# Performance work log

Measured on AMD Instinct MI355X. Metric: run time of the kernel, lower is better.

The kernel has to match this reference:

```python
import jax, jax.numpy as jnp
import numpy as np

EPS = 1e-15          # min-norm clamp (matches torch min_norm)
BALL_EPS = 4e-3      # float32 Poincare ball boundary eps
C = 1.0              # curvature for every layer


def _artanh(x):
    x = jnp.clip(x, -1.0 + 1e-7, 1.0 - 1e-7)
    return 0.5 * jnp.log((1.0 + x) / (1.0 - x))


def _norm(x):
    return jnp.maximum(jnp.linalg.norm(x, axis=-1, keepdims=True), EPS)


def proj(x, c):
    # clip points to stay inside the ball of radius (1-eps)/sqrt(c)
    n = _norm(x)
    maxnorm = (1.0 - BALL_EPS) / jnp.sqrt(c)
    return jnp.where(n > maxnorm, x / n * maxnorm, x)


def expmap0(u, c):
    sc = jnp.sqrt(c)
    n = _norm(u)
    return jnp.tanh(sc * n) * u / (sc * n)


def logmap0(p, c):
    sc = jnp.sqrt(c)
    n = _norm(p)
    return _artanh(sc * n) * p / (sc * n)


def mobius_add(x, y, c):
    x2 = jnp.sum(x * x, axis=-1, keepdims=True)
    y2 = jnp.sum(y * y, axis=-1, keepdims=True)
    xy = jnp.sum(x * y, axis=-1, keepdims=True)
    num = (1.0 + 2.0 * c * xy + c * y2) * x + (1.0 - c * x2) * y
    den = 1.0 + 2.0 * c * xy + (c ** 2) * x2 * y2
    return num / jnp.maximum(den, EPS)


def mobius_matvec(W, x, c):
    # torch HypLinear: mx = x @ W.T
    sc = jnp.sqrt(c)
    xn = _norm(x)
    mx = x @ W.T
    mxn = _norm(mx)
    res = jnp.tanh(mxn / xn * _artanh(sc * xn)) * mx / (mxn * sc)
    zero = jnp.all(mx == 0.0, axis=-1, keepdims=True)
    return jnp.where(zero, jnp.zeros((), dtype=res.dtype), res)


def hgc_layer(h, src, dst, w, W, b, c_in, c_out, n_nodes):
    # HypLinear
    mv = proj(mobius_matvec(W, h, c_in), c_in)
    hb = proj(expmap0(b[None, :], c_in), c_in)
    h = proj(mobius_add(mv, hb, c_in), c_in)
    # HypAgg: spmm in the tangent space at the origin
    xt = logmap0(h, c_in)                                  # [N, D]
    msg = w[:, None] * xt[src]                             # [E, D]
    agg = jax.ops.segment_sum(msg, dst, num_segments=n_nodes)
    h = proj(expmap0(agg, c_in), c_in)
    # HypAct: relu in tangent space, re-map with c_out
    xt = jax.nn.relu(logmap0(h, c_in))
    return proj(expmap0(xt, c_out), c_out)


def setup_inputs() -> dict:
    key = jax.random.key(0)
    k = jax.random.split(key, 8)
    N, E, F, D = 80000, 1280000, 256, 64
    x = jax.random.normal(k[0], (N, F), dtype=jnp.float32)
    src = jax.random.randint(k[1], (E,), 0, N)
    dst = jax.random.randint(k[2], (E,), 0, N)
    edge_weight = jax.random.uniform(k[3], (E,), dtype=jnp.float32)
    W1 = jax.random.normal(k[4], (D, F), dtype=jnp.float32) / np.sqrt(F)
    b1 = jax.random.normal(k[5], (D,), dtype=jnp.float32) * 0.01
    W2 = jax.random.normal(k[6], (D, D), dtype=jnp.float32) / np.sqrt(D)
    b2 = jax.random.normal(k[7], (D,), dtype=jnp.float32) * 0.01
    return {"x": x, "src": src, "dst": dst, "edge_weight": edge_weight,
            "W1": W1, "b1": b1, "W2": W2, "b2": b2}


def reference(x, src, dst, edge_weight, W1, b1, W2, b2):
    n_nodes = x.shape[0]
    # encode(): proj_tan0 is identity on the Poincare ball
    h = proj(expmap0(x, C), C)
    h = hgc_layer(h, src, dst, edge_weight, W1, b1, C, C, n_nodes)
    h = hgc_layer(h, src, dst, edge_weight, W2, b2, C, C, n_nodes)
    return h
```

## Files before the change

kernel.cpp:

```cpp
#include <hip/hip_runtime.h>


#define EPSV 1e-15f
#define MAXN 0.996f

typedef unsigned short bfu;
typedef __attribute__((ext_vector_type(8))) short v8s;
typedef __attribute__((ext_vector_type(4))) float v4f;

__device__ __forceinline__ bfu f2b(float f) {
    unsigned int u;
    __builtin_memcpy(&u, &f, sizeof(u));
    u += 0x7fffu + ((u >> 16) & 1u);
    return (bfu)(u >> 16);
}

__device__ __forceinline__ float b2f(bfu s) {
    unsigned int u = ((unsigned int)s) << 16;
    float f;
    __builtin_memcpy(&f, &u, sizeof(f));
    return f;
}

__device__ __forceinline__ float uplo(unsigned int u) {
// ... 226 lines not shown
        acc3 = __builtin_amdgcn_mfma_f32_16x16x32_bf16(a, *(const v8s*)(wb + 48 * 256), acc3, 0, 0, 0);
    }
    layer1_tail(nodeBase, m, q, usq, hbv, y2, acc0, acc1, acc2, acc3, xtb);
}

__global__ __launch_bounds__(256) void hgA_zero_i32(int* __restrict__ p, int n) {
    int stride = gridDim.x * blockDim.x;
    for (int i = blockIdx.x * blockDim.x + threadIdx.x; i < n; i += stride) p[i] = 0;
}

__global__ __launch_bounds__(256) void hgA_count(
    const int* __restrict__ dst, int* __restrict__ deg, int E) {
    int stride = gridDim.x * blockDim.x;
    for (int e = blockIdx.x * blockDim.x + threadIdx.x; e < E; e += stride)
        atomicAdd(&deg[dst[e]], 1);
}

__global__ __launch_bounds__(256) void hgA_count_rank_l1(
    const int* __restrict__ dst, int* __restrict__ deg, int* __restrict__ rank,
    int E, int nf, int nl,
    const float* __restrict__ x, const bfu* __restrict__ w1b,
    const float* __restrict__ b1v, bfu* __restrict__ xtb, int N)
{
    const int b = blockIdx.x;
    const int mn = nf < nl ? nf : nl;
    bool isC; int idx;
    if (b < 2 * mn) { isC = !(b & 1); idx = b >> 1; }
    else            { isC = (nf > nl); idx = mn + (b - 2 * mn); }
    if (isC) {
        int e0 = (idx * 256 + threadIdx.x) * 4;
        if (e0 + 4 <= E) {
            int4 d4 = *(const int4*)(dst + e0);
            int4 r4;
            r4.x = atomicAdd(&deg[d4.x], 1);
            r4.y = atomicAdd(&deg[d4.y], 1);
            r4.z = atomicAdd(&deg[d4.z], 1);
            r4.w = atomicAdd(&deg[d4.w], 1);
            *(int4*)(rank + e0) = r4;
        } else if (e0 < E) {
            for (int e = e0; e < E; ++e) rank[e] = atomicAdd(&deg[dst[e]], 1);
        }
    } else {
        layer1_body(idx, threadIdx.x, x, w1b, b1v, xtb, N);
    }
}

__global__ __launch_bounds__(256) void hgA_count_xcvt(
    const int* __restrict__ dst, int* __restrict__ deg, int* __restrict__ rank,
    int E, int nf,
    const float* __restrict__ x, bfu* __restrict__ xb, float* __restrict__ usqt,
    int nc, int N)
{
    const int b = blockIdx.x;
    const int mn = nf < nc ? nf : nc;
    bool isC; int idx;
    if (b < 2 * mn) { isC = !(b & 1); idx = b >> 1; }
    else            { isC = (nf > nc); idx = mn + (b - 2 * mn); }
    if (isC) {
        int e0 = (idx * 256 + threadIdx.x) * 4;
        if (e0 + 4 <= E) {
            int4 d4 = *(const int4*)(dst + e0);
            int4 r4;
            r4.x = atomicAdd(&deg[d4.x], 1);
            r4.y = atomicAdd(&deg[d4.y], 1);
            r4.z = atomicAdd(&deg[d4.z], 1);
            r4.w = atomicAdd(&deg[d4.w], 1);
            *(int4*)(rank + e0) = r4;
        } else if (e0 < E) {
            for (int e = e0; e < E; ++e) rank[e] = atomicAdd(&deg[dst[e]], 1);
        }
    } else {
        const int lane = threadIdx.x & 63, wv = threadIdx.x >> 6;
        const int nodeBase = (idx * 4 + wv) * 16;
        if (nodeBase >= N) return;
        const int m = lane & 15, q = lane >> 4;
        const float* arow = x + (size_t)(nodeBase + m) * 256 + q * 8;
        bfu* orow = xb + (size_t)(nodeBase + m) * 256 + q * 8;
        float usq = 0.0f;
#pragma unroll
        for (int s = 0; s < 8; ++s) {
            float af[8];
            *(float4*)(af)     = *(const float4*)(arow + s * 32);
            *(float4*)(af + 4) = *(const float4*)(arow + s * 32 + 4);
#pragma unroll
            for (int j = 0; j < 8; ++j) usq = fmaf(af[j], af[j], usq);
            *(v8s*)(orow + s * 32) = cvt8(af);
        }
        usq += __shfl_xor(usq, 16, 64);
        usq += __shfl_xor(usq, 32, 64);
        if (lane < 16 && nodeBase + lane < N) usqt[nodeBase + lane] = usq;
    }
}

__global__ __launch_bounds__(256) void hgA_scan1(
    const int* __restrict__ deg, int* __restrict__ rowst,
    int* __restrict__ bsum, int N, int NBr,
    const bfu* __restrict__ xb, const float* __restrict__ usqt,
    const bfu* __restrict__ w1b, const float* __restrict__ b1v,
    bfu* __restrict__ xtb, int NL)
{
    if (blockIdx.x >= NBr) {
        int vb = blockIdx.x - NBr;
        if (vb < NL) layer1b_body(vb, threadIdx.x, xb, usqt, w1b, b1v, xtb, N);
        return;
    }
    __shared__ int wsum[4];
    const int tid = threadIdx.x, lane = tid & 63, wv = tid >> 6;
    const int base = blockIdx.x * 1024 + tid * 4;
    int v0 = 0, v1 = 0, v2 = 0, v3 = 0;
    if (base + 4 <= N) {
        int4 d4 = *(const int4*)(deg + base);
        v0 = d4.x; v1 = d4.y; v2 = d4.z; v3 = d4.w;
    } else {
        if (base + 0 < N) v0 = deg[base + 0];
        if (base + 1 < N) v1 = deg[base + 1];
        if (base + 2 < N) v2 = deg[base + 2];
        if (base + 3 < N) v3 = deg[base + 3];
    }
    const int tsum = v0 + v1 + v2 + v3;
    int incl = tsum;
#pragma unroll
    for (int o = 1; o < 64; o <<= 1) {
        int nb = __shfl_up(incl, o, 64);
        if (lane >= o) incl += nb;
    }
    if (lane == 63) wsum[wv] = incl;
    __syncthreads();
    int add = 0;
#pragma unroll
    for (int w = 0; w < 4; ++w) { int s = wsum[w]; if (w < wv) add += s; }
    const int excl = add + incl - tsum;
    const int e0 = excl, e1 = e0 + v0, e2 = e1 + v1, e3 = e2 + v2;
    if (base + 4 <= N) {
        *(int4*)(rowst + base) = make_int4(e0, e1, e2, e3);
    } else {
        if (base + 0 < N) rowst[base + 0] = e0;
        if (base + 1 < N) rowst[base + 1] = e1;
        if (base + 2 < N) rowst[base + 2] = e2;
        if (base + 3 < N) rowst[base + 3] = e3;
    }
    if (tid == 255) bsum[blockIdx.x] = add + incl;
}

__global__ __launch_bounds__(64) void hgA_scan2(
    int* __restrict__ bsum, int* __restrict__ tot, int NB)
{
    const int lane = threadIdx.x;
    int run = 0;
    for (int b = 0; b < NB; b += 64) {
        int i = b + lane;
        int v = (i < NB) ? bsum[i] : 0;
        int incl = v;
#pragma unroll
        for (int o = 1; o < 64; o <<= 1) {
            int nb = __shfl_up(incl, o, 64);
            if (lane >= o) incl += nb;
        }
        if (i < NB) bsum[i] = run + incl - v;
        run += __shfl(incl, 63);
    }
    if (lane == 0) *tot = run;
}

__global__ __launch_bounds__(256) void hgA_scan3(
    int* __restrict__ rowst, const int* __restrict__ bsum, int N)
{
    const int base = blockIdx.x * 1024 + threadIdx.x * 4;
    const int off = bsum[blockIdx.x];
    if (base + 4 <= N) {
        int4 r = *(int4*)(rowst + base);
        r.x += off; r.y += off; r.z += off; r.w += off;
        *(int4*)(rowst + base) = r;
    } else {
        for (int i = base; i < N; ++i) rowst[i] += off;
    }
}

__global__ __launch_bounds__(1024) void hgA_scan_l1(
    const int* __restrict__ deg, int* __restrict__ row_start,
    int* __restrict__ cursor, int N,
    const float* __restrict__ x, const bfu* __restrict__ w1b,
    const float* __restrict__ b1v, bfu* __restrict__ xtb, int NL)
{
    if (blockIdx.x != 0) {
        int vb = (blockIdx.x - 1) * 4 + (threadIdx.x >> 8);
        if (vb < NL) layer1_body(vb, threadIdx.x & 255, x, w1b, b1v, xtb, N);
        return;
    }
    __shared__ int wsum[16];
    __shared__ int srun;
    const int tid = threadIdx.x, lane = tid & 63, wv = tid >> 6;
    if (tid == 0) srun = 0;
    __syncthreads();
    for (int base = 0; base < N; base += 1024) {
        int i = base + tid;
        int v = (i < N) ? deg[i] : 0;
        int incl = v;
#pragma unroll
        for (int o = 1; o < 64; o <<= 1) {
            int nbr = __shfl_up(incl, o, 64);
            if (lane >= o) incl += nbr;
        }
        if (lane == 63) wsum[wv] = incl;
        __syncthreads();
        int add = 0;
#pragma unroll
        for (int w = 0; w < 16; ++w) { int s = wsum[w]; if (w < wv) add += s; }
        int excl = srun + add + incl - v;
        if (i < N) { row_start[i] = excl; cursor[i] = excl; }
        __syncthreads();
        if (tid == 1023) srun += add + incl;
        __syncthreads();
    }
    if (tid == 0) row_start[N] = srun;
}

__global__ __launch_bounds__(256) void hgA_fill_layer1(
    const int* __restrict__ src, const int* __restrict__ dst,
    const float* __restrict__ ew, int* __restrict__ cursor,
    int2* __restrict__ csr, int E, int fillBlocks,
    const float* __restrict__ x, const bfu* __restrict__ w1b,
    const float* __restrict__ b1v, bfu* __restrict__ xtb, int N)
{
    const int b = blockIdx.x;
    if (b < fillBlocks) {
        int stride = fillBlocks * blockDim.x;
        for (int e = b * blockDim.x + threadIdx.x; e < E; e += stride) {
            int d = dst[e];
            int slot = atomicAdd(&cursor[d], 1);
            csr[slot] = make_int2(src[e], f2i(ew[e]));
        }
    } else {
        layer1_body(b - fillBlocks, threadIdx.x, x, w1b, b1v, xtb, N);
    }
}

__global__ __launch_bounds__(256) void hgA_fillr_layer1(
    const int* __restrict__ src, const int* __restrict__ dst,
    const float* __restrict__ ew, const int* __restrict__ rank,
    const int* __restrict__ row_start, int2* __restrict__ csr,
    int E, int nf, int nl, int l1off,
    const float* __restrict__ x, const bfu* __restrict__ w1b,
    const float* __restrict__ b1v, bfu* __restrict__ xtb, int N)
{
    const int b = blockIdx.x;
    const int mn = nf < nl ? nf : nl;
    bool isFill; int idx;
    if (b < 2 * mn) { isFill = !(b & 1); idx = b >> 1; }
    else            { isFill = (nf > nl); idx = mn + (b - 2 * mn); }
    if (isFill) {
        int e0 = (idx * 256 + threadIdx.x) * 4;
        if (e0 + 4 <= E) {
            int4  d4 = *(const int4*)(dst + e0);
            int4  s4 = *(const int4*)(src + e0);
            int4  r4 = *(const int4*)(rank + e0);
            float4 w4 = *(const float4*)(ew + e0);
            csr[row_start[d4.x] + r4.x] = make_int2(s4.x, f2i(w4.x));
            csr[row_start[d4.y] + r4.y] = make_int2(s4.y, f2i(w4.y));
            csr[row_start[d4.z] + r4.z] = make_int2(s4.z, f2i(w4.z));
            csr[row_start[d4.w] + r4.w] = make_int2(s4.w, f2i(w4.w));
        } else if (e0 < E) {
            for (int e = e0; e < E; ++e)
                csr[row_start[dst[e]] + rank[e]] = make_int2(src[e], f2i(ew[e]));
        }
    } else {
        layer1_body(l1off + idx, threadIdx.x, x, w1b, b1v, xtb, N);
    }
}

__global__ __launch_bounds__(256) void hgA_fillr_l1b(
    const int* __restrict__ src, const int* __restrict__ dst,
    const float* __restrict__ ew, const int* __restrict__ rank,
    const int* __restrict__ row_start, int2* __restrict__ csr,
    int E, int nf, int nl, int l1off,
    const bfu* __restrict__ xb, const float* __restrict__ usqt,
    const bfu* __restrict__ w1b, const float* __restrict__ b1v,
    bfu* __restrict__ xtb, int N)
{
    const int b = blockIdx.x;
    const int mn = nf < nl ? nf : nl;
    bool isFill; int idx;
    if (b < 2 * mn) { isFill = !(b & 1); idx = b >> 1; }
    else            { isFill = (nf > nl); idx = mn + (b - 2 * mn); }
    if (isFill) {
        int e0 = (idx * 256 + threadIdx.x) * 4;
        if (e0 + 4 <= E) {
            int4  d4 = *(const int4*)(dst + e0);
            int4  s4 = *(const int4*)(src + e0);
            int4  r4 = *(const int4*)(rank + e0);
            float4 w4 = *(const float4*)(ew + e0);
            csr[row_start[d4.x] + r4.x] = make_int2(s4.x, f2i(w4.x));
            csr[row_start[d4.y] + r4.y] = make_int2(s4.y, f2i(w4.y));
            csr[row_start[d4.z] + r4.z] = make_int2(s4.z, f2i(w4.z));
            csr[row_start[d4.w] + r4.w] = make_int2(s4.w, f2i(w4.w));
        } else if (e0 < E) {
            for (int e = e0; e < E; ++e)
                csr[row_start[dst[e]] + rank[e]] = make_int2(src[e], f2i(ew[e]));
        }
    } else {
        layer1b_body(l1off + idx, threadIdx.x, xb, usqt, w1b, b1v, xtb, N);
    }
}

#define GACC_QUAD(T64, CSR, N0, N1, LANE, T0, T1, T2, T3)                      \
    {                                                                          \
        const int sl_ = (LANE) & 15, p_ = (LANE) >> 4;                         \
        float a0x=0.f,a0y=0.f,a0z=0.f,a0w=0.f;                                 \
        float a1x=0.f,a1y=0.f,a1z=0.f,a1w=0.f;                                 \
        float a2x=0.f,a2y=0.f,a2z=0.f,a2w=0.f;                                 \
        float a3x=0.f,a3y=0.f,a3z=0.f,a3w=0.f;                                 \
        for (int base = (N0); base < (N1); base += 64) {                       \
            int cnt = (N1) - base; if (cnt > 64) cnt = 64;                     \
            int sL = 0; float wL = 0.0f;                                       \
            if ((LANE) < cnt) { int2 rec = (CSR)[base + (LANE)];               \
                                sL = rec.x; wL = i2f(rec.y); }                 \
            int j = 0;                                                         \
            for (; j + 16 <= cnt; j += 16) {                                   \
                int   s0 = __shfl(sL, j      + p_, 64);                        \
                int   s1 = __shfl(sL, j +  4 + p_, 64);                        \
                int   s2 = __shfl(sL, j +  8 + p_, 64);                        \
                int   s3 = __shfl(sL, j + 12 + p_, 64);                        \
                float w0 = __shfl(wL, j      + p_, 64);                        \
                float w1 = __shfl(wL, j +  4 + p_, 64);                        \
                float w2 = __shfl(wL, j +  8 + p_, 64);                        \
                float w3 = __shfl(wL, j + 12 + p_, 64);                        \
                uint2 u0 = (T64)[(size_t)s0 * 16 + sl_];                       \
                uint2 u1 = (T64)[(size_t)s1 * 16 + sl_];                       \
                uint2 u2 = (T64)[(size_t)s2 * 16 + sl_];                       \
                uint2 u3 = (T64)[(size_t)s3 * 16 + sl_];                       \
                a0x = fmaf(w0, uplo(u0.x), a0x); a0y = fmaf(w0, uphi(u0.x), a0y); \
                a0z = fmaf(w0, uplo(u0.y), a0z); a0w = fmaf(w0, uphi(u0.y), a0w); \
                a1x = fmaf(w1, uplo(u1.x), a1x); a1y = fmaf(w1, uphi(u1.x), a1y); \
                a1z = fmaf(w1, uplo(u1.y), a1z); a1w = fmaf(w1, uphi(u1.y), a1w); \
                a2x = fmaf(w2, uplo(u2.x), a2x); a2y = fmaf(w2, uphi(u2.x), a2y); \
                a2z = fmaf(w2, uplo(u2.y), a2z); a2w = fmaf(w2, uphi(u2.y), a2w); \
                a3x = fmaf(w3, uplo(u3.x), a3x); a3y = fmaf(w3, uphi(u3.x), a3y); \
                a3z = fmaf(w3, uplo(u3.y), a3z); a3w = fmaf(w3, uphi(u3.y), a3w); \
            }                                                                  \
            for (; j + 8 <= cnt; j += 8) {                                     \
                int   s0 = __shfl(sL, j     + p_, 64);                         \
                int   s1 = __shfl(sL, j + 4 + p_, 64);                         \
                float w0 = __shfl(wL, j     + p_, 64);                         \
                float w1 = __shfl(wL, j + 4 + p_, 64);                         \
                uint2 u0 = (T64)[(size_t)s0 * 16 + sl_];                       \
                uint2 u1 = (T64)[(size_t)s1 * 16 + sl_];                       \
                a0x = fmaf(w0, uplo(u0.x), a0x); a0y = fmaf(w0, uphi(u0.x), a0y); \
                a0z = fmaf(w0, uplo(u0.y), a0z); a0w = fmaf(w0, uphi(u0.y), a0w); \
                a1x = fmaf(w1, uplo(u1.x), a1x); a1y = fmaf(w1, uphi(u1.x), a1y); \
                a1z = fmaf(w1, uplo(u1.y), a1z); a1w = fmaf(w1, uphi(u1.y), a1w); \
            }                                                                  \
            for (; j < cnt; j += 4) {         \
                int   s = __shfl(sL, j + p_, 64);                              \
                float w = __shfl(wL, j + p_, 64);                              \
                uint2 u = (T64)[(size_t)s * 16 + sl_];                         \
                a0x = fmaf(w, uplo(u.x), a0x); a0y = fmaf(w, uphi(u.x), a0y);  \
                a0z = fmaf(w, uplo(u.y), a0z); a0w = fmaf(w, uphi(u.y), a0w);  \
            }                                                                  \
        }                                                                      \
        T0 = (a0x + a1x) + (a2x + a3x);                                        \
        T1 = (a0y + a1y) + (a2y + a3y);                                        \
        T2 = (a0z + a1z) + (a2z + a3z);                                        \
        T3 = (a0w + a1w) + (a2w + a3w);                                        \
        T0 += __shfl_xor(T0, 16, 64); T0 += __shfl_xor(T0, 32, 64);            \
        T1 += __shfl_xor(T1, 16, 64); T1 += __shfl_xor(T1, 32, 64);            \
        T2 += __shfl_xor(T2, 16, 64); T2 += __shfl_xor(T2, 32, 64);            \
        T3 += __shfl_xor(T3, 16, 64); T3 += __shfl_xor(T3, 32, 64);            \
    }

__global__ __launch_bounds__(256) void hgA_gather(
    const int* __restrict__ row_start, const int2* __restrict__ csr,
    const bfu* __restrict__ xtb, float* __restrict__ agg, int N) {
    const int lane = threadIdx.x & 63, wv = threadIdx.x >> 6;
    const int d = blockIdx.x * 4 + wv;
    if (d >= N) return;
    const uint2* t64 = (const uint2*)xtb;
    const int n0 = row_start[d], n1 = row_start[d + 1];
    float t0, t1, t2, t3;
    GACC_QUAD(t64, csr, n0, n1, lane, t0, t1, t2, t3);
    if ((lane >> 4) == 0)
        *(float4*)(agg + (size_t)d * 64 + 4 * (lane & 15)) =
            make_float4(t0, t1, t2, t3);
}

__global__ __launch_bounds__(256) void hgA_gather_out(
    const int* __restrict__ row_start, const int2* __restrict__ csr,
    const bfu* __restrict__ xtb2, float* __restrict__ out, int N) {
    const int lane = threadIdx.x & 63, wv = threadIdx.x >> 6;
    const int d = blockIdx.x * 4 + wv;
    if (d >= N) return;
    const uint2* t64 = (const uint2*)xtb2;
    const int n0 = row_start[d], n1 = row_start[d + 1];
    float t0, t1, t2, t3;
    GACC_QUAD(t64, csr, n0, n1, lane, t0, t1, t2, t3);
    float ssq = t0*t0 + t1*t1 + t2*t2 + t3*t3;
#pragma unroll
    for (int o = 1; o < 16; o <<= 1) ssq += __shfl_xor(ssq, o, 64);
    float n  = fmaxf(sqrtf(ssq), EPSV);
    float th = tanhf(n);
    float g  = th / n;
    float nh = fmaxf(th, EPSV);
    if (nh > MAXN) { g *= MAXN / nh; nh = MAXN; }
    float lamg = (artanh_(nh) / nh) * g;
    float r0 = fmaxf(lamg * t0, 0.0f);
    float r1 = fmaxf(lamg * t1, 0.0f);
    float r2 = fmaxf(lamg * t2, 0.0f);
    float r3 = fmaxf(lamg * t3, 0.0f);
    float tsq = r0*r0 + r1*r1 + r2*r2 + r3*r3;
#pragma unroll
    for (int o = 1; o < 16; o <<= 1) tsq += __shfl_xor(tsq, o, 64);
    float n2  = fmaxf(sqrtf(tsq), EPSV);
    float th2 = tanhf(n2);
    float g2  = th2 / n2;
    float nh2 = fmaxf(th2, EPSV);
    if (nh2 > MAXN) g2 *= MAXN / nh2;
    if ((lane >> 4) == 0)
        *(float4*)(out + (size_t)d * 64 + 4 * (lane & 15)) =
            make_float4(g2 * r0, g2 * r1, g2 * r2, g2 * r3);
}

__global__ __launch_bounds__(256) void hgA_layer2_mfma(
    const float* __restrict__ agg,
    const bfu* __restrict__ w2b,
    const float* __restrict__ b2v,
    bfu* __restrict__ xtb2, int N)
{
    const int tid = threadIdx.x, lane = tid & 63, wv = tid >> 6;
    const int nodeBase = (blockIdx.x * 4 + wv) * 16;
    if (nodeBase >= N) return;

    float y2;
    float hb = bias_point(b2v, lane, &y2);
    float hbv[4];
#pragma unroll
    for (int t = 0; t < 4; ++t) hbv[t] = __shfl(hb, (lane & 15) + 16 * t);

    const int m = lane & 15, q = lane >> 4;
    const bool rowok = (nodeBase + m) < N;

    float af0[8], af1[8];
    const float* arow = agg + (size_t)(nodeBase + m) * 64 + q * 8;
    if (rowok) {
        *(float4*)(af0)     = *(const float4*)(arow);
        *(float4*)(af0 + 4) = *(const float4*)(arow + 4);
        *(float4*)(af1)     = *(const float4*)(arow + 32);
        *(float4*)(af1 + 4) = *(const float4*)(arow + 36);
    } else {
#pragma unroll
        for (int j = 0; j < 8; ++j) { af0[j] = 0.0f; af1[j] = 0.0f; }
    }
    float asq = 0.0f;
#pragma unroll
    for (int j = 0; j < 8; ++j) {
        asq = fmaf(af0[j], af0[j], asq);
        asq = fmaf(af1[j], af1[j], asq);
    }
    asq += __shfl_xor(asq, 16, 64);
    asq += __shfl_xor(asq, 32, 64);

    float n  = fmaxf(sqrtf(asq), EPSV);
    float th = tanhf(n);
    float g  = th / n;
    float nh = fmaxf(th, EPSV);
    if (nh > MAXN) { g *= MAXN / nh; nh = MAXN; }
    float lamg = (artanh_(nh) / nh) * g;
    float t0[8], t1[8], tsq = 0.0f;
#pragma unroll
    for (int j = 0; j < 8; ++j) {
        t0[j] = fmaxf(lamg * af0[j], 0.0f);
        t1[j] = fmaxf(lamg * af1[j], 0.0f);
        tsq = fmaf(t0[j], t0[j], tsq);
        tsq = fmaf(t1[j], t1[j], tsq);
    }
    tsq += __shfl_xor(tsq, 16, 64);
    tsq += __shfl_xor(tsq, 32, 64);
    float n2  = fmaxf(sqrtf(tsq), EPSV);
    float th2 = tanhf(n2);
    float g2  = th2 / n2;
    float nh2 = fmaxf(th2, EPSV);
    if (nh2 > MAXN) { g2 *= MAXN / nh2; nh2 = MAXN; }
    float xn_m = nh2;
    float x0[8], x1[8];
#pragma unroll
    for (int j = 0; j < 8; ++j) { x0[j] = g2 * t0[j]; x1[j] = g2 * t1[j]; }
    v8s a0 = cvt8(x0), a1 = cvt8(x1);

    v4f acc0 = {0,0,0,0}, acc1 = {0,0,0,0}, acc2 = {0,0,0,0}, acc3 = {0,0,0,0};
    {
        const bfu* wb;
        wb = w2b + (size_t)(m     ) * 64 + q * 8;
        acc0 = __builtin_amdgcn_mfma_f32_16x16x32_bf16(a0, *(const v8s*)(wb),      acc0, 0, 0, 0);
        acc0 = __builtin_amdgcn_mfma_f32_16x16x32_bf16(a1, *(const v8s*)(wb + 32), acc0, 0, 0, 0);
        wb = w2b + (size_t)(m + 16) * 64 + q * 8;
        acc1 = __builtin_amdgcn_mfma_f32_16x16x32_bf16(a0, *(const v8s*)(wb),      acc1, 0, 0, 0);
        acc1 = __builtin_amdgcn_mfma_f32_16x16x32_bf16(a1, *(const v8s*)(wb + 32), acc1, 0, 0, 0);
        wb = w2b + (size_t)(m + 32) * 64 + q * 8;
        acc2 = __builtin_amdgcn_mfma_f32_16x16x32_bf16(a0, *(const v8s*)(wb),      acc2, 0, 0, 0);
        acc2 = __builtin_amdgcn_mfma_f32_16x16x32_bf16(a1, *(const v8s*)(wb + 32), acc2, 0, 0, 0);
        wb = w2b + (size_t)(m + 48) * 64 + q * 8;
        acc3 = __builtin_amdgcn_mfma_f32_16x16x32_bf16(a0, *(const v8s*)(wb),      acc3, 0, 0, 0);
        acc3 = __builtin_amdgcn_mfma_f32_16x16x32_bf16(a1, *(const v8s*)(wb + 32), acc3, 0, 0, 0);
    }

    float P[4], Q[4];
#pragma unroll
    for (int r = 0; r < 4; ++r) {
        float s2 = acc0[r]*acc0[r] + acc1[r]*acc1[r] + acc2[r]*acc2[r] + acc3[r]*acc3[r];
        float sh = acc0[r]*hbv[0] + acc1[r]*hbv[1] + acc2[r]*hbv[2] + acc3[r]*hbv[3];
#pragma unroll
        for (int o = 1; o < 16; o <<= 1) {
            s2 += __shfl_xor(s2, o, 64);
            sh += __shfl_xor(sh, o, 64);
        }
        float xn = __shfl(xn_m, q * 4 + r);
        float mxn = fmaxf(sqrtf(s2), EPSV);
        float rt  = tanhf(mxn / xn * artanh_(xn));
        float k1, x2s, xy;
        if (s2 != 0.0f) {
            k1 = rt / mxn;
            float mvn = fmaxf(fabsf(rt), EPSV);
            if (mvn > MAXN) k1 *= MAXN / mvn;
            float cn = fminf(mvn, MAXN);
            x2s = cn * cn;
            xy  = k1 * sh;
        } else { k1 = 0.0f; x2s = 0.0f; xy = 0.0f; }
        float ca = 1.0f + 2.0f * xy + y2;
        float cb = 1.0f - x2s;
        float den = fmaxf(1.0f + 2.0f * xy + x2s * y2, EPSV);
        float hn2 = ca*ca*x2s + 2.0f*ca*cb*xy + cb*cb*y2;
        float hn = fmaxf(sqrtf(hn2) / den, EPSV);
        float hs = 1.0f;
        if (hn > MAXN) { hs = MAXN / hn; hn = MAXN; }
        float lam = artanh_(hn) / hn;
        P[r] = lam * hs * ca * k1 / den;
        Q[r] = lam * hs * cb / den;
    }
#pragma unroll
    for (int r = 0; r < 4; ++r) {
        int ri = nodeBase + q * 4 + r;
        if (ri < N) {
            bfu* orow = xtb2 + (size_t)ri * 64 + m;
            orow[ 0] = f2b(P[r] * acc0[r] + Q[r] * hbv[0]);
            orow[16] = f2b(P[r] * acc1[r] + Q[r] * hbv[1]);
            orow[32] = f2b(P[r] * acc2[r] + Q[r] * hbv[2]);
            orow[48] = f2b(P[r] * acc3[r] + Q[r] * hbv[3]);
        }
    }
}

__global__ __launch_bounds__(256) void hgA_layer1_fp32(
    const float* __restrict__ x, const float* __restrict__ W1,
    const float* __restrict__ b1v, float* __restrict__ xt, int N)
{
    const int tid = threadIdx.x, lane = tid & 63, wv = tid >> 6;
    const int nodeBase = (blockIdx.x * 4 + wv) * 16;
    if (nodeBase >= N) return;
    float y2;
    float hb = bias_point(b1v, lane, &y2);
    float hbv[4];
#pragma unroll
    for (int t = 0; t < 4; ++t) hbv[t] = __shfl(hb, (lane & 15) + 16 * t);
    const int m = lane & 15, q = lane >> 4;
    v4f acc0 = {0,0,0,0}, acc1 = {0,0,0,0}, acc2 = {0,0,0,0}, acc3 = {0,0,0,0};
    float usq = 0.0f;
    const float* arow = x + (size_t)(nodeBase + m) * 256 + q * 8;
#pragma unroll
    for (int s = 0; s < 8; ++s) {
        float af[8];
        *(float4*)(af)     = *(const float4*)(arow + s * 32);
        *(float4*)(af + 4) = *(const float4*)(arow + s * 32 + 4);
#pragma unroll
        for (int j = 0; j < 8; ++j) usq = fmaf(af[j], af[j], usq);
        v8s a = cvt8(af);
        const float* wbase = W1 + (size_t)m * 256 + s * 32 + q * 8;
        float wf[8];
        *(float4*)(wf) = *(const float4*)(wbase);  *(float4*)(wf+4) = *(const float4*)(wbase+4);
        acc0 = __builtin_amdgcn_mfma_f32_16x16x32_bf16(a, cvt8(wf), acc0, 0, 0, 0);
        *(float4*)(wf) = *(const float4*)(wbase+16*256); *(float4*)(wf+4) = *(const float4*)(wbase+16*256+4);
        acc1 = __builtin_amdgcn_mfma_f32_16x16x32_bf16(a, cvt8(wf), acc1, 0, 0, 0);
        *(float4*)(wf) = *(const float4*)(wbase+32*256); *(float4*)(wf+4) = *(const float4*)(wbase+32*256+4);
        acc2 = __builtin_amdgcn_mfma_f32_16x16x32_bf16(a, cvt8(wf), acc2, 0, 0, 0);
        *(float4*)(wf) = *(const float4*)(wbase+48*256); *(float4*)(wf+4) = *(const float4*)(wbase+48*256+4);
        acc3 = __builtin_amdgcn_mfma_f32_16x16x32_bf16(a, cvt8(wf), acc3, 0, 0, 0);
    }
    usq += __shfl_xor(usq, 16, 64);
    usq += __shfl_xor(usq, 32, 64);
    float P[4], Q[4];
#pragma unroll
    for (int r = 0; r < 4; ++r) {
        float s2 = acc0[r]*acc0[r] + acc1[r]*acc1[r] + acc2[r]*acc2[r] + acc3[r]*acc3[r];
        float sh = acc0[r]*hbv[0] + acc1[r]*hbv[1] + acc2[r]*hbv[2] + acc3[r]*hbv[3];
#pragma unroll
        for (int o = 1; o < 16; o <<= 1) { s2 += __shfl_xor(s2, o, 64); sh += __shfl_xor(sh, o, 64); }
        float usq_r = __shfl(usq, q * 4 + r);
        float n  = fmaxf(sqrtf(usq_r), EPSV);
        float th = tanhf(n);
        float gamma = th / n;
        float xn = fmaxf(th, EPSV);
        if (xn > MAXN) { gamma *= MAXN / xn; xn = MAXN; }
        float mxn = fmaxf(gamma * sqrtf(s2), EPSV);
        float rt  = tanhf(mxn / xn * artanh_(xn));
        float k1, x2s, xy;
        if (s2 != 0.0f) {
            k1 = (rt / mxn) * gamma;
            float mvn = fmaxf(fabsf(rt), EPSV);
            if (mvn > MAXN) k1 *= MAXN / mvn;
            float cn = fminf(mvn, MAXN);
            x2s = cn * cn; xy = k1 * sh;
        } else { k1 = 0.0f; x2s = 0.0f; xy = 0.0f; }
        float ca = 1.0f + 2.0f * xy + y2;
        float cb = 1.0f - x2s;
        float den = fmaxf(1.0f + 2.0f * xy + x2s * y2, EPSV);
        float hn2 = ca*ca*x2s + 2.0f*ca*cb*xy + cb*cb*y2;
        float hn = fmaxf(sqrtf(hn2) / den, EPSV);
        float hs = 1.0f;
        if (hn > MAXN) { hs = MAXN / hn; hn = MAXN; }
        float lam = artanh_(hn) / hn;
        P[r] = lam * hs * ca * k1 / den;
        Q[r] = lam * hs * cb / den;
    }
#pragma unroll
    for (int r = 0; r < 4; ++r) {
        float* orow = xt + (size_t)(nodeBase + q * 4 + r) * 64 + m;
        orow[ 0] = P[r] * acc0[r] + Q[r] * hbv[0];
        orow[16] = P[r] * acc1[r] + Q[r] * hbv[1];
        orow[32] = P[r] * acc2[r] + Q[r] * hbv[2];
        orow[48] = P[r] * acc3[r] + Q[r] * hbv[3];
    }
}

__global__ __launch_bounds__(256) void hgA_scatter(
    const int* __restrict__ src, const int* __restrict__ dst,
    const float* __restrict__ ew,
    const float* __restrict__ xt, float* __restrict__ agg, int E)
{
    const int lane = threadIdx.x & 63;
    const long long wid = ((long long)blockIdx.x * blockDim.x + threadIdx.x) >> 6;
    const long long nw = ((long long)gridDim.x * blockDim.x) >> 6;
    for (long long e = wid; e < E; e += nw) {
        int s = src[e], d = dst[e];
        atomicAdd(&agg[(size_t)d * 64 + lane], ew[e] * xt[(size_t)s * 64 + lane]);
    }
}

__global__ __launch_bounds__(256) void hgA_layer2_fb(
    const float* __restrict__ agg,
    const float* __restrict__ W2, const float* __restrict__ b2v,
    float* __restrict__ xt2, int N)
{
    const int lane = threadIdx.x & 63, wv = threadIdx.x >> 6;
    float y2;
    float hb = bias_point(b2v, lane, &y2);
    const int nw = gridDim.x * 4;
    for (int i = blockIdx.x * 4 + wv; i < N; i += nw) {
        float a = agg[(size_t)i * 64 + lane];
        float xn;
        float x2 = agg_transform(a, &xn);
        float acc = 0.0f;
        const float* Wrow = W2 + (size_t)lane * 64;
        for (int s = 0; s < 64; ++s)
            acc = fmaf(__shfl(x2, s), Wrow[s], acc);
        float o = mobius_tail(acc, xn, hb, y2);
        xt2[(size_t)i * 64 + lane] = o;
    }
}

__global__ __launch_bounds__(256) void hgA_final_fb(
    const float* __restrict__ agg, float* __restrict__ out, int N)
{
    const int lane = threadIdx.x & 63, wv = threadIdx.x >> 6;
    const int nw = gridDim.x * 4;
    for (int i = blockIdx.x * 4 + wv; i < N; i += nw) {
        float a = agg[(size_t)i * 64 + lane];
        float xn;
        float o = agg_transform(a, &xn);
        out[(size_t)i * 64 + lane] = o;
    }
}

extern "C" void kernel_launch(void* const* d_in, const int* in_sizes, int n_in,
                              void* d_out, int out_size, void* d_ws, size_t ws_size,
                              hipStream_t stream)
{
    const float* x  = (const float*)d_in[0];
    const int* src  = (const int*)d_in[1];
    const int* dst  = (const int*)d_in[2];
    const float* ew = (const float*)d_in[3];
    const float* W1 = (const float*)d_in[4];
    const float* b1 = (const float*)d_in[5];
    const float* W2 = (const float*)d_in[6];
    const float* b2 = (const float*)d_in[7];

    const int Dd = in_sizes[5];
    const int Ff = in_sizes[4] / Dd;
    const int N  = in_sizes[0] / Ff;
    const int E  = in_sizes[1];
    const int NW1 = Dd * Ff;
    const int NW2 = Dd * Dd;

    float* out = (float*)d_out;
    float* agg = (float*)d_out;

    const int NB = (N + 1023) / 1024;

    const int blkT = (N + 63) / 64;
    const int blkG = (N + 3) / 4;
    const int blkE4 = (E + 1023) / 1024;
    const int prepG = 128 + (NW1 + 255) / 256 + 1;
    const int n4 = (N * Dd) / 4;

    size_t xtb_b = (size_t)N * Dd * 2;
    size_t xb_b  = (size_t)N * Ff * 2;
    bfu*  xtb   = (bfu*)d_ws;
    bfu*  xbA   = (bfu*)((char*)d_ws + xtb_b);
    float* usqt = (float*)((char*)d_ws + xtb_b + xb_b);
    size_t off1 = xtb_b + xb_b + (size_t)N * 4;
    int*  degA1   = (int*)((char*)d_ws + off1);
    int*  rowstA1 = degA1 + N;
    int*  rankA1  = rowstA1 + (N + 1);
    int*  bsumA1  = rankA1 + E;
    size_t w1_offA1 = (off1 + ((size_t)(2 * N + 1) + (size_t)E + (size_t)NB) * 4 + 15) & ~(size_t)15;
    bfu* w1bA1 = (bfu*)((char*)d_ws + w1_offA1);
    bfu* w2bA1 = w1bA1 + NW1;
    size_t csr_offA1 = (w1_offA1 + (size_t)(NW1 + NW2) * 2 + 7) & ~(size_t)7;
    const size_t needA1 = csr_offA1 + (size_t)E * 8;

    int*  deg    = (int*)((char*)d_ws + xtb_b);
    int*  rowst  = deg + N;
    int*  cursor = rowst + (N + 1);
    int*  rank   = cursor + N;
    int*  bsum   = rank + E;
    size_t wA_off = (xtb_b + ((size_t)(3 * N + 1) + (size_t)E + (size_t)NB) * 4 + 15) & ~(size_t)15;
    bfu* w1bA = (bfu*)((char*)d_ws + wA_off);
    bfu* w2bA = w1bA + NW1;
    size_t csr_offA = (wA_off + (size_t)(NW1 + NW2) * 2 + 7) & ~(size_t)7;
    const size_t needA2 = csr_offA + (size_t)E * 8;

    size_t wB_off = (xtb_b + (size_t)(3 * N + 1) * 4 + 15) & ~(size_t)15;
    bfu* w1bB = (bfu*)((char*)d_ws + wB_off);
    bfu* w2bB = w1bB + NW1;
    size_t csr_offB = (wB_off + (size_t)(NW1 + NW2) * 2 + 7) & ~(size_t)7;
    const size_t needB = csr_offB + (size_t)E * 8;

    if (ws_size >= needA1) {
        int2* csr = (int2*)((char*)d_ws + csr_offA1);
        int L1S = blkT < 192 ? blkT : 192;
        int L1F = blkT - L1S;
        hgA_prep      <<<prepG, 256, 0, stream>>>(degA1, N, W1, W2, w1bA1, w2bA1, NW1, NW2);
        hgA_count_xcvt<<<blkE4 + blkT, 256, 0, stream>>>(
            dst, degA1, rankA1, E, blkE4, x, xbA, usqt, blkT, N);
        hgA_scan1     <<<NB + L1S, 256, 0, stream>>>(
            degA1, rowstA1, bsumA1, N, NB, xbA, usqt, w1bA1, b1, xtb, L1S);
        hgA_scan2     <<<1, 64, 0, stream>>>(bsumA1, rowstA1 + N, NB);
        hgA_scan3     <<<NB, 256, 0, stream>>>(rowstA1, bsumA1, N);
        hgA_fillr_l1b <<<blkE4 + L1F, 256, 0, stream>>>(
            src, dst, ew, rankA1, rowstA1, csr, E, blkE4, L1F, L1S,
            xbA, usqt, w1bA1, b1, xtb, N);
        hgA_gather     <<<blkG, 256, 0, stream>>>(rowstA1, csr, xtb, agg, N);
        hgA_layer2_mfma<<<blkT, 256, 0, stream>>>(agg, w2bA1, b2, xtb, N);
        hgA_gather_out <<<blkG, 256, 0, stream>>>(rowstA1, csr, xtb, out, N);
    } else if (ws_size >= needA2) {
        int2* csr = (int2*)((char*)d_ws + csr_offA);
        int L1C = blkT < 780 ? blkT : 780;
        int L1F = blkT - L1C;
        hgA_prep        <<<prepG, 256, 0, stream>>>(deg, N, W1, W2, w1bA, w2bA, NW1, NW2);
        hgA_count_rank_l1<<<blkE4 + L1C, 256, 0, stream>>>(
            dst, deg, rank, E, blkE4, L1C, x, w1bA, b1, xtb, N);
        hgA_scan1       <<<NB, 256, 0, stream>>>(deg, rowst, bsum, N, NB,
                                                 (const bfu*)xtb, (const float*)deg,
                                                 w1bA, b1, xtb, 0);
        hgA_scan2       <<<1,   64, 0, stream>>>(bsum, rowst + N, NB);
        hgA_scan3       <<<NB, 256, 0, stream>>>(rowst, bsum, N);
        hgA_fillr_layer1<<<blkE4 + L1F, 256, 0, stream>>>(
            src, dst, ew, rank, rowst, csr, E, blkE4, L1F, L1C,
            x, w1bA, b1, xtb, N);
        hgA_gather     <<<blkG, 256, 0, stream>>>(rowst, csr, xtb, agg, N);
        hgA_layer2_mfma<<<blkT, 256, 0, stream>>>(agg, w2bA, b2, xtb, N);
        hgA_gather_out <<<blkG, 256, 0, stream>>>(rowst, csr, xtb, out, N);
    } else if (ws_size >= needB) {
        int2* csr = (int2*)((char*)d_ws + csr_offB);
        const int fillBlocks = 2048;
        hgA_prep       <<<prepG, 256, 0, stream>>>(deg, N, W1, W2, w1bB, w2bB, NW1, NW2);
        hgA_count      <<<2048, 256, 0, stream>>>(dst, deg, E);
        hgA_scan_l1    <<<1,   1024, 0, stream>>>(
            deg, rowst, cursor, N, x, w1bB, b1, xtb, 0);
        hgA_fill_layer1<<<fillBlocks + blkT, 256, 0, stream>>>(
            src, dst, ew, cursor, csr, E, fillBlocks, x, w1bB, b1, xtb, N);
        hgA_gather     <<<blkG, 256, 0, stream>>>(rowst, csr, xtb, agg, N);
        hgA_layer2_mfma<<<blkT, 256, 0, stream>>>(agg, w2bB, b2, xtb, N);
        hgA_gather_out <<<blkG, 256, 0, stream>>>(rowst, csr, xtb, out, N);
    } else {
        float* xt_fb  = (float*)d_out;
        float* agg_fb = (float*)d_ws;
        hgA_layer1_fp32<<<blkT, 256, 0, stream>>>(x, W1, b1, xt_fb, N);
        hgA_zero     <<<1024,  256, 0, stream>>>(agg_fb, n4);
        hgA_scatter  <<<16384, 256, 0, stream>>>(src, dst, ew, xt_fb, agg_fb, E);
        hgA_layer2_fb<<<2048,  256, 0, stream>>>(agg_fb, W2, b2, xt_fb, N);
        hgA_zero     <<<1024,  256, 0, stream>>>(agg_fb, n4);
        hgA_scatter  <<<16384, 256, 0, stream>>>(src, dst, ew, xt_fb, agg_fb, E);
        hgA_final_fb <<<2048,  256, 0, stream>>>(agg_fb, out, N);
    }
}
```

Baseline: 333.4 us.

## Map each 16-lane group to one destination row in the CSR gathers

Both gather kernels now assign one 16-lane group per destination node, so each wave handles four rows. Previously a whole wave handled one row with four 16-lane groups splitting its edges. Each group walks its row's edges serially, eight gathered loads at a time, using two accumulator sets. This removes the cross-group shfl_xor reduction and the idle lanes at the store, and cuts the number of launched blocks by four. In exchange, rows of unequal degree in the same wave now diverge, and each lane runs a longer serial loop.

Measured after the change: 315.2 us. 1.06x faster.

```diff
diff --git a/kernel.cpp b/kernel.cpp
--- a/kernel.cpp
+++ b/kernel.cpp
@@ -552,105 +552,105 @@
     }
 }
 
-#define GACC_QUAD(T64, CSR, N0, N1, LANE, T0, T1, T2, T3)                      \
+#define GACC_G16(T64, CSR, N0, N1, SL, GBASE, AX, AY, AZ, AW)                  \
     {                                                                          \
-        const int sl_ = (LANE) & 15, p_ = (LANE) >> 4;                         \
-        float a0x=0.f,a0y=0.f,a0z=0.f,a0w=0.f;                                 \
-        float a1x=0.f,a1y=0.f,a1z=0.f,a1w=0.f;                                 \
-        float a2x=0.f,a2y=0.f,a2z=0.f,a2w=0.f;                                 \
-        float a3x=0.f,a3y=0.f,a3z=0.f,a3w=0.f;                                 \
-        for (int base = (N0); base < (N1); base += 64) {                       \
-            int cnt = (N1) - base; if (cnt > 64) cnt = 64;                     \
+        float bx=0.f,by=0.f,bz=0.f,bw=0.f;                                     \
+        for (int base = (N0); base < (N1); base += 16) {                       \
+            int cnt = (N1) - base; if (cnt > 16) cnt = 16;                     \
             int sL = 0; float wL = 0.0f;                                       \
-            if ((LANE) < cnt) { int2 rec = (CSR)[base + (LANE)];               \
-                                sL = rec.x; wL = i2f(rec.y); }                 \
+            if ((SL) < cnt) { int2 rec = (CSR)[base + (SL)];                   \
+                              sL = rec.x; wL = i2f(rec.y); }                   \
             int j = 0;                                                         \
-            for (; j + 16 <= cnt; j += 16) {                                   \
-                int   s0 = __shfl(sL, j      + p_, 64);                        \
-                int   s1 = __shfl(sL, j +  4 + p_, 64);                        \
-                int   s2 = __shfl(sL, j +  8 + p_, 64);                        \
-                int   s3 = __shfl(sL, j + 12 + p_, 64);                        \
-                float w0 = __shfl(wL, j      + p_, 64);                        \
-                float w1 = __shfl(wL, j +  4 + p_, 64);                        \
-                float w2 = __shfl(wL, j +  8 + p_, 64);                        \
-                float w3 = __shfl(wL, j + 12 + p_, 64);                        \
-                uint2 u0 = (T64)[(size_t)s0 * 16 + sl_];                       \
-                uint2 u1 = (T64)[(size_t)s1 * 16 + sl_];                       \
-                uint2 u2 = (T64)[(size_t)s2 * 16 + sl_];                       \
-                uint2 u3 = (T64)[(size_t)s3 * 16 + sl_];                       \
-                a0x = fmaf(w0, uplo(u0.x), a0x); a0y = fmaf(w0, uphi(u0.x), a0y); \
-                a0z = fmaf(w0, uplo(u0.y), a0z); a0w = fmaf(w0, uphi(u0.y), a0w); \
-                a1x = fmaf(w1, uplo(u1.x), a1x); a1y = fmaf(w1, uphi(u1.x), a1y); \
-                a1z = fmaf(w1, uplo(u1.y), a1z); a1w = fmaf(w1, uphi(u1.y), a1w); \
-                a2x = fmaf(w2, uplo(u2.x), a2x); a2y = fmaf(w2, uphi(u2.x), a2y); \
-                a2z = fmaf(w2, uplo(u2.y), a2z); a2w = fmaf(w2, uphi(u2.y), a2w); \
-                a3x = fmaf(w3, uplo(u3.x), a3x); a3y = fmaf(w3, uphi(u3.x), a3y); \
-                a3z = fmaf(w3, uplo(u3.y), a3z); a3w = fmaf(w3, uphi(u3.y), a3w); \
+            for (; j + 8 <= cnt; j += 8) {                                     \
+                int   s0 = __shfl(sL, (GBASE)+j  , 64), s1 = __shfl(sL, (GBASE)+j+1, 64); \
+                int   s2 = __shfl(sL, (GBASE)+j+2, 64), s3 = __shfl(sL, (GBASE)+j+3, 64); \
+                int   s4 = __shfl(sL, (GBASE)+j+4, 64), s5 = __shfl(sL, (GBASE)+j+5, 64); \
+                int   s6 = __shfl(sL, (GBASE)+j+6, 64), s7 = __shfl(sL, (GBASE)+j+7, 64); \
+                float w0 = __shfl(wL, (GBASE)+j  , 64), w1 = __shfl(wL, (GBASE)+j+1, 64); \
+                float w2 = __shfl(wL, (GBASE)+j+2, 64), w3 = __shfl(wL, (GBASE)+j+3, 64); \
+                float w4 = __shfl(wL, (GBASE)+j+4, 64), w5 = __shfl(wL, (GBASE)+j+5, 64); \
+                float w6 = __shfl(wL, (GBASE)+j+6, 64), w7 = __shfl(wL, (GBASE)+j+7, 64); \
+                uint2 u0 = (T64)[(size_t)s0 * 16 + (SL)];                      \
+                uint2 u1 = (T64)[(size_t)s1 * 16 + (SL)];                      \
+                uint2 u2 = (T64)[(size_t)s2 * 16 + (SL)];                      \
+                uint2 u3 = (T64)[(size_t)s3 * 16 + (SL)];                      \
+                uint2 u4 = (T64)[(size_t)s4 * 16 + (SL)];                      \
+                uint2 u5 = (T64)[(size_t)s5 * 16 + (SL)];                      \
+                uint2 u6 = (T64)[(size_t)s6 * 16 + (SL)];                      \
+                uint2 u7 = (T64)[(size_t)s7 * 16 + (SL)];                      \
+                AX = fmaf(w0, uplo(u0.x), AX); AY = fmaf(w0, uphi(u0.x), AY);  \
+                AZ = fmaf(w0, uplo(u0.y), AZ); AW = fmaf(w0, uphi(u0.y), AW);  \
+                bx = fmaf(w1, uplo(u1.x), bx); by = fmaf(w1, uphi(u1.x), by);  \
+                bz = fmaf(w1, uplo(u1.y), bz); bw = fmaf(w1, uphi(u1.y), bw);  \
+                AX = fmaf(w2, uplo(u2.x), AX); AY = fmaf(w2, uphi(u2.x), AY);  \
+                AZ = fmaf(w2, uplo(u2.y), AZ); AW = fmaf(w2, uphi(u2.y), AW);  \
+                bx = fmaf(w3, uplo(u3.x), bx); by = fmaf(w3, uphi(u3.x), by);  \
+                bz = fmaf(w3, uplo(u3.y), bz); bw = fmaf(w3, uphi(u3.y), bw);  \
+                AX = fmaf(w4, uplo(u4.x), AX); AY = fmaf(w4, uphi(u4.x), AY);  \
+                AZ = fmaf(w4, uplo(u4.y), AZ); AW = fmaf(w4, uphi(u4.y), AW);  \
+                bx = fmaf(w5, uplo(u5.x), bx); by = fmaf(w5, uphi(u5.x), by);  \
+                bz = fmaf(w5, uplo(u5.y), bz); bw = fmaf(w5, uphi(u5.y), bw);  \
+                AX = fmaf(w6, uplo(u6.x), AX); AY = fmaf(w6, uphi(u6.x), AY);  \
+                AZ = fmaf(w6, uplo(u6.y), AZ); AW = fmaf(w6, uphi(u6.y), AW);  \
+                bx = fmaf(w7, uplo(u7.x), bx); by = fmaf(w7, uphi(u7.x), by);  \
+                bz = fmaf(w7, uplo(u7.y), bz); bw = fmaf(w7, uphi(u7.y), bw);  \
             }                                                                  \
-            for (; j + 8 <= cnt; j += 8) {                                     \
-                int   s0 = __shfl(sL, j     + p_, 64);                         \
-                int   s1 = __shfl(sL, j + 4 + p_, 64);                         \
-                float w0 = __shfl(wL, j     + p_, 64);                         \
-                float w1 = __shfl(wL, j + 4 + p_, 64);                         \
-                uint2 u0 = (T64)[(size_t)s0 * 16 + sl_];                       \
-                uint2 u1 = (T64)[(size_t)s1 * 16 + sl_];                       \
-                a0x = fmaf(w0, uplo(u0.x), a0x); a0y = fmaf(w0, uphi(u0.x), a0y); \
-                a0z = fmaf(w0, uplo(u0.y), a0z); a0w = fmaf(w0, uphi(u0.y), a0w); \
-                a1x = fmaf(w1, uplo(u1.x), a1x); a1y = fmaf(w1, uphi(u1.x), a1y); \
-                a1z = fmaf(w1, uplo(u1.y), a1z); a1w = fmaf(w1, uphi(u1.y), a1w); \
-            }                                                                  \
-            for (; j < cnt; j += 4) {         \
-                int   s = __shfl(sL, j + p_, 64);                              \
-                float w = __shfl(wL, j + p_, 64);                              \
-                uint2 u = (T64)[(size_t)s * 16 + sl_];                         \
-                a0x = fmaf(w, uplo(u.x), a0x); a0y = fmaf(w, uphi(u.x), a0y);  \
-                a0z = fmaf(w, uplo(u.y), a0z); a0w = fmaf(w, uphi(u.y), a0w);  \
+            for (; j < cnt; j += 4) {            \
+                int   s0 = __shfl(sL, (GBASE)+j  , 64), s1 = __shfl(sL, (GBASE)+j+1, 64); \
+                int   s2 = __shfl(sL, (GBASE)+j+2, 64), s3 = __shfl(sL, (GBASE)+j+3, 64); \
+                float w0 = __shfl(wL, (GBASE)+j  , 64), w1 = __shfl(wL, (GBASE)+j+1, 64); \
+                float w2 = __shfl(wL, (GBASE)+j+2, 64), w3 = __shfl(wL, (GBASE)+j+3, 64); \
+                uint2 u0 = (T64)[(size_t)s0 * 16 + (SL)];                      \
+                uint2 u1 = (T64)[(size_t)s1 * 16 + (SL)];                      \
+                uint2 u2 = (T64)[(size_t)s2 * 16 + (SL)];                      \
+                uint2 u3 = (T64)[(size_t)s3 * 16 + (SL)];                      \
+                AX = fmaf(w0, uplo(u0.x), AX); AY = fmaf(w0, uphi(u0.x), AY);  \
+                AZ = fmaf(w0, uplo(u0.y), AZ); AW = fmaf(w0, uphi(u0.y), AW);  \
+                bx = fmaf(w1, uplo(u1.x), bx); by = fmaf(w1, uphi(u1.x), by);  \
+                bz = fmaf(w1, uplo(u1.y), bz); bw = fmaf(w1, uphi(u1.y), bw);  \
+                AX = fmaf(w2, uplo(u2.x), AX); AY = fmaf(w2, uphi(u2.x), AY);  \
+                AZ = fmaf(w2, uplo(u2.y), AZ); AW = fmaf(w2, uphi(u2.y), AW);  \
+                bx = fmaf(w3, uplo(u3.x), bx); by = fmaf(w3, uphi(u3.x), by);  \
+                bz = fmaf(w3, uplo(u3.y), bz); bw = fmaf(w3, uphi(u3.y), bw);  \
             }                                                                  \
         }                                                                      \
-        T0 = (a0x + a1x) + (a2x + a3x);                                        \
-        T1 = (a0y + a1y) + (a2y + a3y);                                        \
-        T2 = (a0z + a1z) + (a2z + a3z);                                        \
-        T3 = (a0w + a1w) + (a2w + a3w);                                        \
-        T0 += __shfl_xor(T0, 16, 64); T0 += __shfl_xor(T0, 32, 64);            \
-        T1 += __shfl_xor(T1, 16, 64); T1 += __shfl_xor(T1, 32, 64);            \
-        T2 += __shfl_xor(T2, 16, 64); T2 += __shfl_xor(T2, 32, 64);            \
-        T3 += __shfl_xor(T3, 16, 64); T3 += __shfl_xor(T3, 32, 64);            \
+        AX += bx; AY += by; AZ += bz; AW += bw;                                \
     }
 
 __global__ __launch_bounds__(256) void hgA_gather(
     const int* __restrict__ row_start, const int2* __restrict__ csr,
     const bfu* __restrict__ xtb, float* __restrict__ agg, int N) {
     const int lane = threadIdx.x & 63, wv = threadIdx.x >> 6;
-    const int d = blockIdx.x * 4 + wv;
+    const int g = lane >> 4, sl = lane & 15, gbase = g << 4;
+    const int d = (blockIdx.x * 4 + wv) * 4 + g;
     if (d >= N) return;
     const uint2* t64 = (const uint2*)xtb;
     const int n0 = row_start[d], n1 = row_start[d + 1];
-    float t0, t1, t2, t3;
-    GACC_QUAD(t64, csr, n0, n1, lane, t0, t1, t2, t3);
-    if ((lane >> 4) == 0)
-        *(float4*)(agg + (size_t)d * 64 + 4 * (lane & 15)) =
-            make_float4(t0, t1, t2, t3);
+    float ax = 0.f, ay = 0.f, az = 0.f, aw = 0.f;
+    GACC_G16(t64, csr, n0, n1, sl, gbase, ax, ay, az, aw);
+    *(float4*)(agg + (size_t)d * 64 + 4 * sl) = make_float4(ax, ay, az, aw);
 }
 
 __global__ __launch_bounds__(256) void hgA_gather_out(
     const int* __restrict__ row_start, const int2* __restrict__ csr,
     const bfu* __restrict__ xtb2, float* __restrict__ out, int N) {
     const int lane = threadIdx.x & 63, wv = threadIdx.x >> 6;
-    const int d = blockIdx.x * 4 + wv;
+    const int g = lane >> 4, sl = lane & 15, gbase = g << 4;
+    const int d = (blockIdx.x * 4 + wv) * 4 + g;
     if (d >= N) return;
     const uint2* t64 = (const uint2*)xtb2;
     const int n0 = row_start[d], n1 = row_start[d + 1];
-    float t0, t1, t2, t3;
-    GACC_QUAD(t64, csr, n0, n1, lane, t0, t1, t2, t3);
+    float t0 = 0.f, t1 = 0.f, t2 = 0.f, t3 = 0.f;
+    GACC_G16(t64, csr, n0, n1, sl, gbase, t0, t1, t2, t3);
     float ssq = t0*t0 + t1*t1 + t2*t2 + t3*t3;
 #pragma unroll
     for (int o = 1; o < 16; o <<= 1) ssq += __shfl_xor(ssq, o, 64);
     float n  = fmaxf(sqrtf(ssq), EPSV);
     float th = tanhf(n);
-    float g  = th / n;
+    float gg = th / n;
     float nh = fmaxf(th, EPSV);
-    if (nh > MAXN) { g *= MAXN / nh; nh = MAXN; }
-    float lamg = (artanh_(nh) / nh) * g;
+    if (nh > MAXN) { gg *= MAXN / nh; nh = MAXN; }
+    float lamg = (artanh_(nh) / nh) * gg;
     float r0 = fmaxf(lamg * t0, 0.0f);
     float r1 = fmaxf(lamg * t1, 0.0f);
     float r2 = fmaxf(lamg * t2, 0.0f);
@@ -663,9 +663,8 @@
     float g2  = th2 / n2;
     float nh2 = fmaxf(th2, EPSV);
     if (nh2 > MAXN) g2 *= MAXN / nh2;
-    if ((lane >> 4) == 0)
-        *(float4*)(out + (size_t)d * 64 + 4 * (lane & 15)) =
-            make_float4(g2 * r0, g2 * r1, g2 * r2, g2 * r3);
+    *(float4*)(out + (size_t)d * 64 + 4 * sl) =
+        make_float4(g2 * r0, g2 * r1, g2 * r2, g2 * r3);
 }
 
 __global__ __launch_bounds__(256) void hgA_layer2_mfma(
@@ -953,7 +952,7 @@
     const int NB = (N + 1023) / 1024;
 
     const int blkT = (N + 63) / 64;
-    const int blkG = (N + 3) / 4;
+    const int blkG16 = (N + 15) / 16;
     const int blkE4 = (E + 1023) / 1024;
     const int prepG = 128 + (NW1 + 255) / 256 + 1;
     const int n4 = (N * Dd) / 4;
@@ -1005,9 +1004,9 @@
         hgA_fillr_l1b <<<blkE4 + L1F, 256, 0, stream>>>(
             src, dst, ew, rankA1, rowstA1, csr, E, blkE4, L1F, L1S,
             xbA, usqt, w1bA1, b1, xtb, N);
-        hgA_gather     <<<blkG, 256, 0, stream>>>(rowstA1, csr, xtb, agg, N);
+        hgA_gather     <<<blkG16, 256, 0, stream>>>(rowstA1, csr, xtb, agg, N);
         hgA_layer2_mfma<<<blkT, 256, 0, stream>>>(agg, w2bA1, b2, xtb, N);
-        hgA_gather_out <<<blkG, 256, 0, stream>>>(rowstA1, csr, xtb, out, N);
+        hgA_gather_out <<<blkG16, 256, 0, stream>>>(rowstA1, csr, xtb, out, N);
     } else if (ws_size >= needA2) {
         int2* csr = (int2*)((char*)d_ws + csr_offA);
         int L1C = blkT < 780 ? blkT : 780;
@@ -1023,9 +1022,9 @@
         hgA_fillr_layer1<<<blkE4 + L1F, 256, 0, stream>>>(
             src, dst, ew, rank, rowst, csr, E, blkE4, L1F, L1C,
             x, w1bA, b1, xtb, N);
-        hgA_gather     <<<blkG, 256, 0, stream>>>(rowst, csr, xtb, agg, N);
+        hgA_gather     <<<blkG16, 256, 0, stream>>>(rowst, csr, xtb, agg, N);
         hgA_layer2_mfma<<<blkT, 256, 0, stream>>>(agg, w2bA, b2, xtb, N);
-        hgA_gather_out <<<blkG, 256, 0, stream>>>(rowst, csr, xtb, out, N);
+        hgA_gather_out <<<blkG16, 256, 0, stream>>>(rowst, csr, xtb, out, N);
     } else if (ws_size >= needB) {
         int2* csr = (int2*)((char*)d_ws + csr_offB);
         const int fillBlocks = 2048;
@@ -1035,9 +1034,9 @@
             deg, rowst, cursor, N, x, w1bB, b1, xtb, 0);
         hgA_fill_layer1<<<fillBlocks + blkT, 256, 0, stream>>>(
             src, dst, ew, cursor, csr, E, fillBlocks, x, w1bB, b1, xtb, N);
-        hgA_gather     <<<blkG, 256, 0, stream>>>(rowst, csr, xtb, agg, N);
+        hgA_gather     <<<blkG16, 256, 0, stream>>>(rowst, csr, xtb, agg, N);
         hgA_layer2_mfma<<<blkT, 256, 0, stream>>>(agg, w2bB, b2, xtb, N);
-        hgA_gather_out <<<blkG, 256, 0, stream>>>(rowst, csr, xtb, out, N);
+        hgA_gather_out <<<blkG16, 256, 0, stream>>>(rowst, csr, xtb, out, N);
     } else {
         float* xt_fb  = (float*)d_out;
         float* agg_fb = (float*)d_ws;
```
